# Kernel optimization log

Measured on AMD Instinct MI355X. Metric: run time of the kernel, lower is better.

Reference implementation:

```python
import jax, jax.numpy as jnp
import numpy as np

APPERTURE = 256
Q_SCALE = 0.06


def setup_inputs() -> dict:
    key = jax.random.key(0)
    ks = jax.random.split(key, 5)
    B, N, D_IN, D_OUT = 4, 4096, 1024, 1024
    std = 1.0 / np.sqrt(D_IN)
    x = jax.random.normal(ks[0], (B, N, D_IN), dtype=jnp.float32)
    Wk = jax.random.normal(ks[1], (D_OUT, D_IN), dtype=jnp.float32) * std
    Wq = jax.random.normal(ks[2], (D_OUT, D_IN), dtype=jnp.float32) * std
    Wv = jax.random.normal(ks[3], (D_OUT, D_IN), dtype=jnp.float32) * std
    Wo = jax.random.normal(ks[4], (D_IN, D_OUT), dtype=jnp.float32) * std
    return {"x": x, "Wk": Wk, "Wq": Wq, "Wv": Wv, "Wo": Wo}


def reference(x, Wk, Wq, Wv, Wo):
    # x: [B, N, D_in]; torch Linear(W) computes x @ W.T
    K = jnp.einsum('bnd,od->bno', x, Wk)          # [B, N, D_out]
    Q = jnp.einsum('bnd,od->bno', x, Wq) * Q_SCALE
    V = jnp.einsum('bnd,od->bno', x, Wv)
    logits = jnp.einsum('bno,bmo->bnm', Q, K)      # [B, N, N]
    N = x.shape[1]
    idx = jnp.arange(N)
    # tril(-a) + triu(a) masks |i-j| >= apperture (keep strict band)
    band_mask = jnp.abs(idx[:, None] - idx[None, :]) >= APPERTURE  # [N, N]
    logits = jnp.where(band_mask[None, :, :], -jnp.inf, logits)
    att_weights = jax.nn.softmax(logits, axis=-1)  # [B, N, N]
    # dropout is identity in eval mode
    # y = (V^T @ weights)^T  ->  y[b,n,:] = sum_m att[b,m,n] * V[b,m,:]
    y = jnp.einsum('bmn,bmo->bno', att_weights, V)
    y = jnp.einsum('bno,io->bni', y, Wo)           # [B, N, D_in]
    return (y, att_weights)
```

## Files before the change

kernel.cpp:

```cpp
#include <hip/hip_runtime.h>
#include <stdint.h>

#define SEQ 4096
#define DM  1024
#define NB  4
#define QSCALE 0.06f

typedef __attribute__((ext_vector_type(8))) short short8;
typedef __attribute__((ext_vector_type(4))) float floatx4;

__device__ __forceinline__ unsigned short f2bf(float f) {
  union { float f; unsigned int u; } v; v.f = f;
  unsigned int u = v.u;
  u += 0x7FFFu + ((u >> 16) & 1u);
  return (unsigned short)(u >> 16);
}

__device__ __forceinline__ void async16(const void* g, void* l) {
  __builtin_amdgcn_global_load_lds(
      (const __attribute__((address_space(1))) void*)g,
      (__attribute__((address_space(3))) void*)l, 16, 0, 0);
}

__global__ void cvt_bf16(const float* __restrict__ in,
                         unsigned short* __restrict__ out, int n) {
  int i = (blockIdx.x * 256 + threadIdx.x) * 8;
  if (i >= n) return;
  const float4* p = (const float4*)(in + i);
  float4 a = p[0], b = p[1];
  short8 o;
  o[0] = (short)f2bf(a.x); o[1] = (short)f2bf(a.y);
  o[2] = (short)f2bf(a.z); o[3] = (short)f2bf(a.w);
  o[4] = (short)f2bf(b.x); o[5] = (short)f2bf(b.y);
  o[6] = (short)f2bf(b.z); o[7] = (short)f2bf(b.w);
  *(short8*)(out + i) = o;
}

template <bool OUT_BF16, int MT>
__global__ __launch_bounds__(512, 2) void gemm256(
    const unsigned short* __restrict__ A, const unsigned short* __restrict__ W,
    void* __restrict__ Cout, float alpha, long ldc) {
  __shared__ __align__(16) unsigned short lds[4 * 16384];
  const int K = 1024;
  const int NKT = 32;
  int tid = threadIdx.x;
  int lane = tid & 63;
  int wid = tid >> 6;
  int wr = wid >> 2, wc = wid & 3;

  int bid = blockIdx.x;
  int raw = ((bid & 7) << 5) | (bid >> 3);
  int bx = raw % MT;
  int by = raw / MT;
  long brow = (long)bx * 256;
  long bcol = (long)by * 256;

  floatx4 acc[8][4];
#pragma unroll
  for (int i = 0; i < 8; i++)
#pragma unroll
    for (int j = 0; j < 4; j++) acc[i][j] = (floatx4){0.f, 0.f, 0.f, 0.f};

  const unsigned short* Ag = A + (brow + (tid >> 2)) * K + (tid & 3) * 8;
  const unsigned short* Wg = W + (bcol + (tid >> 2)) * K + (tid & 3) * 8;
  unsigned short* ldsW = lds + wid * 512;

  int aRd = (wr * 128 + (lane & 15)) * 32 + (lane >> 4) * 8;
  int bRd = (wc * 64 + (lane & 15)) * 32 + (lane >> 4) * 8;

#pragma unroll
  for (int tt = 0; tt < 3; tt++) {
    unsigned short* d = ldsW + tt * 16384;
    const unsigned short* a = Ag + tt * 32;
    const unsigned short* w = Wg + tt * 32;
    async16(a, d);
    async16(a + 128 * K, d + 4096);
    async16(w, d + 8192);
    async16(w + 128 * K, d + 12288);
  }
  asm volatile("s_waitcnt vmcnt(8)" ::: "memory");
  __builtin_amdgcn_s_barrier();

  for (int t = 0; t < NKT; ++t) {
    const unsigned short* bufA = lds + (t & 3) * 16384;
    const unsigned short* bufB = bufA + 8192;
    short8 a0[4], b0[4], a1[4];
#pragma unroll
    for (int mt = 0; mt < 4; mt++)
      a0[mt] = *(const short8*)(bufA + aRd + mt * 512);
#pragma unroll
    for (int nt = 0; nt < 4; nt++)
      b0[nt] = *(const short8*)(bufB + bRd + nt * 512);
    if (t + 3 < NKT) {
      unsigned short* d = ldsW + ((t + 3) & 3) * 16384;
      const unsigned short* a = Ag + (t + 3) * 32;
      async16(a, d);
      async16(a + 128 * K, d + 4096);
    }
    __builtin_amdgcn_s_barrier();
    __builtin_amdgcn_s_setprio(1);
#pragma unroll
    for (int mt = 0; mt < 4; mt++)
#pragma unroll
      for (int nt = 0; nt < 4; nt++)
        acc[mt][nt] = __builtin_amdgcn_mfma_f32_16x16x32_bf16(
            a0[mt], b0[nt], acc[mt][nt], 0, 0, 0);
    __builtin_amdgcn_s_setprio(0);
    __builtin_amdgcn_s_barrier();
#pragma unroll
    for (int mt = 0; mt < 4; mt++)
      a1[mt] = *(const short8*)(bufA + aRd + 2048 + mt * 512);
    if (t + 3 < NKT) {
      unsigned short* d = ldsW + ((t + 3) & 3) * 16384;
      const unsigned short* w = Wg + (t + 3) * 32;
      async16(w, d + 8192);
      async16(w + 128 * K, d + 12288);
    }
    __builtin_amdgcn_s_barrier();
    __builtin_amdgcn_s_setprio(1);
#pragma unroll
    for (int mt = 0; mt < 4; mt++)
#pragma unroll
      for (int nt = 0; nt < 4; nt++)
        acc[4 + mt][nt] = __builtin_amdgcn_mfma_f32_16x16x32_bf16(
            a1[mt], b0[nt], acc[4 + mt][nt], 0, 0, 0);
    __builtin_amdgcn_s_setprio(0);
    if (t < NKT - 3)
      asm volatile("s_waitcnt vmcnt(8)" ::: "memory");
    else if (t == NKT - 3)
      asm volatile("s_waitcnt vmcnt(4)" ::: "memory");
    else
      asm volatile("s_waitcnt vmcnt(0)" ::: "memory");
    __builtin_amdgcn_s_barrier();
  }

  long crow = brow + wr * 128 + (lane >> 4) * 4;
  long ccol = bcol + wc * 64 + (lane & 15);
#pragma unroll
  for (int mt = 0; mt < 8; mt++)
#pragma unroll
    for (int nt = 0; nt < 4; nt++)
#pragma unroll
      for (int r = 0; r < 4; r++) {
        float v = acc[mt][nt][r] * alpha;
        long idx = (crow + mt * 16 + r) * ldc + ccol + nt * 16;
        if (OUT_BF16)
          ((unsigned short*)Cout)[idx] = f2bf(v);
        else
          ((float*)Cout)[idx] = v;
      }
}

__global__ __launch_bounds__(256) void attn_logits(
    const unsigned short* __restrict__ Qb, const unsigned short* __restrict__ Kb,
    float* __restrict__ att) {
  int b = blockIdx.z;
  int n0 = blockIdx.y * 128;
  int m0 = n0 - 256 + blockIdx.x * 128;
  if (m0 + 128 <= 0 || m0 >= SEQ) return;
  __shared__ unsigned short sA[128 * 32];
  __shared__ unsigned short sB[128 * 32];
  const int K = 1024;
  int tid = threadIdx.x;
  int wid = tid >> 6, lane = tid & 63;
  int wr = wid >> 1, wc = wid & 1;

  floatx4 acc[4][4];
#pragma unroll
  for (int i = 0; i < 4; i++)
#pragma unroll
    for (int j = 0; j < 4; j++) acc[i][j] = (floatx4){0.f, 0.f, 0.f, 0.f};

  int c0 = wid * 64 + lane;
  int c1 = c0 + 256;
  const unsigned short* Qbase = Qb + (long)b * SEQ * K;
  const unsigned short* Kbase = Kb + (long)b * SEQ * K;
  int br0 = m0 + (c0 >> 2); br0 = br0 < 0 ? 0 : (br0 > SEQ - 1 ? SEQ - 1 : br0);
  int br1 = m0 + (c1 >> 2); br1 = br1 < 0 ? 0 : (br1 > SEQ - 1 ? SEQ - 1 : br1);
  const unsigned short* Ag0 = Qbase + (long)(n0 + (c0 >> 2)) * K + (c0 & 3) * 8;
  const unsigned short* Ag1 = Qbase + (long)(n0 + (c1 >> 2)) * K + (c1 & 3) * 8;
  const unsigned short* Bg0 = Kbase + (long)br0 * K + (c0 & 3) * 8;
  const unsigned short* Bg1 = Kbase + (long)br1 * K + (c1 & 3) * 8;
  unsigned short* sA0 = sA + (wid * 64) * 8;
  unsigned short* sA1 = sA + (256 + wid * 64) * 8;
  unsigned short* sB0 = sB + (wid * 64) * 8;
  unsigned short* sB1 = sB + (256 + wid * 64) * 8;

  int aRd = (wr * 64 + (lane & 15)) * 32 + (lane >> 4) * 8;
  int bRd = (wc * 64 + (lane & 15)) * 32 + (lane >> 4) * 8;

  for (int ks = 0; ks < K; ks += 32) {
    async16(Ag0 + ks, sA0);
    async16(Ag1 + ks, sA1);
    async16(Bg0 + ks, sB0);
    async16(Bg1 + ks, sB1);
    __syncthreads();
    short8 af[4], bf[4];
#pragma unroll
    for (int mt = 0; mt < 4; mt++) af[mt] = *(const short8*)(sA + aRd + mt * 512);
#pragma unroll
    for (int nt = 0; nt < 4; nt++) bf[nt] = *(const short8*)(sB + bRd + nt * 512);
#pragma unroll
    for (int mt = 0; mt < 4; mt++)
#pragma unroll
      for (int nt = 0; nt < 4; nt++)
        acc[mt][nt] = __builtin_amdgcn_mfma_f32_16x16x32_bf16(
            af[mt], bf[nt], acc[mt][nt], 0, 0, 0);
    __syncthreads();
  }

  float* attB = att + (long)b * SEQ * SEQ;
  int crow = n0 + wr * 64 + (lane >> 4) * 4;
  int ccol = m0 + wc * 64 + (lane & 15);
#pragma unroll
  for (int mt = 0; mt < 4; mt++)
#pragma unroll
    for (int nt = 0; nt < 4; nt++)
#pragma unroll
      for (int r = 0; r < 4; r++) {
        int row = crow + mt * 16 + r;
        int col = ccol + nt * 16;
        int d = row - col;
        if (col >= 0 && col < SEQ && d < 256 && d > -256)
          attB[(long)row * SEQ + col] = acc[mt][nt][r];
      }
}

__global__ __launch_bounds__(256) void softmax_band(
    float* __restrict__ att, unsigned short* __restrict__ attT2) {
  __shared__ float e_lds[16 * 545];
  __shared__ float inv_s[16];
  int blk = blockIdx.x;
  int b = blk >> 8;
  int r0 = (blk & 255) * 16;
  int tid = threadIdx.x;
  int row = tid >> 4;
  int t16 = tid & 15;
  int i = r0 + row;
  int jbase = r0 - 272;
  float* arow = att + ((long)b * SEQ + i) * (long)SEQ;

  float raw[34];
  float m = -1e30f;
#pragma unroll
  for (int s = 0; s < 34; s++) {
    int jj = s * 16 + t16;
    int j = jbase + jj;
    bool ok = (j >= 0) && (j < SEQ) && (j >= i - 255) && (j <= i + 255);
    float v = ok ? arow[j] : -1e30f;
    raw[s] = v;
    m = fmaxf(m, v);
  }
#pragma unroll
  for (int off = 8; off; off >>= 1) m = fmaxf(m, __shfl_xor(m, off, 16));

  float sum = 0.f;
#pragma unroll
  for (int s = 0; s < 34; s++) {
    int jj = s * 16 + t16;
    float e = (raw[s] > -1e29f) ? __expf(raw[s] - m) : 0.f;
    e_lds[row * 545 + jj] = e;
    sum += e;
  }
#pragma unroll
  for (int off = 8; off; off >>= 1) sum += __shfl_xor(sum, off, 16);
  float invr = 1.0f / sum;
  if (t16 == 0) inv_s[row] = invr;
  __syncthreads();

  for (int s = 0; s < 64; s++) {
    int j0 = (s * 16 + t16) * 4;
    float4 w;
    float* wp = (float*)&w;
#pragma unroll
    for (int k = 0; k < 4; k++) {
      int j = j0 + k;
      bool ok = (j >= i - 255) && (j <= i + 255);
      int jj = j - jbase;
      jj = jj < 0 ? 0 : (jj > 543 ? 543 : jj);
      wp[k] = ok ? e_lds[row * 545 + jj] * invr : 0.f;
    }
    *(float4*)(arow + j0) = w;
  }

  int nn = tid >> 4;
  int mi16 = tid & 15;
  int i2 = r0 + mi16;
  float inv2 = inv_s[mi16];
  for (int s = 0; s <= 32; s++) {
    int n = r0 - 256 + s * 16 + nn;
    if (n < 0 || n >= SEQ) continue;
    int N0b = n & ~127;
    int mi = i2 - N0b + 256;
    if (mi < 0 || mi >= 640) continue;
    bool ok = (n >= i2 - 255) && (n <= i2 + 255);
    int jj = n - jbase;
    float val = ok ? e_lds[mi16 * 545 + jj] * inv2 : 0.f;
    attT2[(((long)b * 32 + (N0b >> 7)) * 128 + (n & 127)) * 640 + mi] = f2bf(val);
  }
}

__global__ __launch_bounds__(256) void attv_gemm(
    const unsigned short* __restrict__ attT2, const unsigned short* __restrict__ Vt,
    unsigned short* __restrict__ yb) {
  __shared__ unsigned short sA[128 * 32];
  __shared__ unsigned short sB[128 * 32];
  const int KA = 640;
  int b = blockIdx.z;
  int tid = threadIdx.x;
  int wid = tid >> 6, lane = tid & 63;
  int wr = wid >> 1, wc = wid & 1;
  int N0 = blockIdx.x * 128;
  int o0 = blockIdx.y * 128;

  floatx4 acc[4][4];
#pragma unroll
  for (int i = 0; i < 4; i++)
#pragma unroll
    for (int j = 0; j < 4; j++) acc[i][j] = (floatx4){0.f, 0.f, 0.f, 0.f};

  int c0 = wid * 64 + lane;
  int c1 = c0 + 256;
  const unsigned short* Abase =
      attT2 + (((long)b * 32 + blockIdx.x) * 128) * KA;
  const unsigned short* Ag0 = Abase + (long)(c0 >> 2) * KA + (c0 & 3) * 8;
  const unsigned short* Ag1 = Abase + (long)(c1 >> 2) * KA + (c1 & 3) * 8;
  const unsigned short* Bg0 = Vt + (long)(o0 + (c0 >> 2)) * (NB * SEQ) + (c0 & 3) * 8;
  const unsigned short* Bg1 = Vt + (long)(o0 + (c1 >> 2)) * (NB * SEQ) + (c1 & 3) * 8;
  unsigned short* sA0 = sA + (wid * 64) * 8;
  unsigned short* sA1 = sA + (256 + wid * 64) * 8;
  unsigned short* sB0 = sB + (wid * 64) * 8;
  unsigned short* sB1 = sB + (256 + wid * 64) * 8;

  int aRd = (wr * 64 + (lane & 15)) * 32 + (lane >> 4) * 8;
  int bRd = (wc * 64 + (lane & 15)) * 32 + (lane >> 4) * 8;

  for (int ks = 0; ks < KA; ks += 32) {
    int mg = N0 - 256 + ks;
    int mc = mg < 0 ? 0 : (mg > SEQ - 32 ? SEQ - 32 : mg);
    long boff = (long)b * SEQ + mc;
    async16(Ag0 + ks, sA0);
    async16(Ag1 + ks, sA1);
    async16(Bg0 + boff, sB0);
    async16(Bg1 + boff, sB1);
    __syncthreads();
    short8 af[4], bf[4];
#pragma unroll
    for (int mt = 0; mt < 4; mt++) af[mt] = *(const short8*)(sA + aRd + mt * 512);
#pragma unroll
    for (int nt = 0; nt < 4; nt++) bf[nt] = *(const short8*)(sB + bRd + nt * 512);
#pragma unroll
    for (int mt = 0; mt < 4; mt++)
#pragma unroll
      for (int nt = 0; nt < 4; nt++)
        acc[mt][nt] = __builtin_amdgcn_mfma_f32_16x16x32_bf16(
            af[mt], bf[nt], acc[mt][nt], 0, 0, 0);
    __syncthreads();
  }

  long crow = (long)b * SEQ + N0 + wr * 64 + (lane >> 4) * 4;
  int ccol = o0 + wc * 64 + (lane & 15);
#pragma unroll
  for (int mt = 0; mt < 4; mt++)
#pragma unroll
    for (int nt = 0; nt < 4; nt++)
#pragma unroll
      for (int r = 0; r < 4; r++)
        yb[(crow + mt * 16 + r) * DM + ccol + nt * 16] = f2bf(acc[mt][nt][r]);
}

extern "C" void kernel_launch(void* const* d_in, const int* in_sizes, int n_in,
                              void* d_out, int out_size, void* d_ws, size_t ws_size,
                              hipStream_t stream) {
  const float* x  = (const float*)d_in[0];
  const float* Wk = (const float*)d_in[1];
  const float* Wq = (const float*)d_in[2];
  const float* Wv = (const float*)d_in[3];
  const float* Wo = (const float*)d_in[4];
  float* outY = (float*)d_out;
  float* outAtt = outY + (long)NB * SEQ * DM;

  char* ws = (char*)d_ws;
  unsigned short* xb  = (unsigned short*)(ws + 0);
  unsigned short* Kb  = (unsigned short*)(ws + 33554432);
  unsigned short* Qb  = (unsigned short*)(ws + 67108864);
  unsigned short* Vt  = (unsigned short*)(ws + 100663296);
  unsigned short* Wkb = (unsigned short*)(ws + 134217728);
  unsigned short* Wqb = Wkb + 1048576;
  unsigned short* Wvb = Wqb + 1048576;
  unsigned short* Wob = Wvb + 1048576;
  unsigned short* attT2 = Kb;
  unsigned short* yb = xb;

  cvt_bf16<<<8192, 256, 0, stream>>>(x, xb, NB * SEQ * DM);
  cvt_bf16<<<512, 256, 0, stream>>>(Wk, Wkb, DM * DM);
  cvt_bf16<<<512, 256, 0, stream>>>(Wq, Wqb, DM * DM);
  cvt_bf16<<<512, 256, 0, stream>>>(Wv, Wvb, DM * DM);
  cvt_bf16<<<512, 256, 0, stream>>>(Wo, Wob, DM * DM);

  gemm256<true, 64><<<256, 512, 0, stream>>>(xb, Wkb, Kb, 1.0f, 1024);
  gemm256<true, 64><<<256, 512, 0, stream>>>(xb, Wqb, Qb, QSCALE, 1024);
  gemm256<true, 4><<<256, 512, 0, stream>>>(Wvb, xb, Vt, 1.0f, NB * SEQ);

  attn_logits<<<dim3(5, 32, NB), 256, 0, stream>>>(Qb, Kb, outAtt);
  hipMemsetAsync(attT2, 0, (size_t)NB * 32 * 128 * 640 * 2, stream);
  softmax_band<<<1024, 256, 0, stream>>>(outAtt, attT2);
  attv_gemm<<<dim3(32, 8, NB), 256, 0, stream>>>(attT2, Vt, yb);
  gemm256<false, 64><<<256, 512, 0, stream>>>(yb, Wob, outY, 1.0f, 1024);
}
```

Measured before the change: 688.7 us.

## Fuse weight conversions and K/Q GEMMs; retile att·V to pipelined 256 blocks

Merges the four weight bf16 conversions into one launch and computes K and Q in a single GEMM over concatenated Wk|Wq, routing output columns to the right buffer with its own scale. Replaces the 128x128 single-buffered att·V GEMM with a 256x256, 512-thread, 4-stage async-pipelined kernel. The transposed attention layout changes to 256-row blocks with a 768-wide band, which adds about 20% more padded K-work per block. The intent is to cut launch overhead and improve MFMA utilisation and data reuse.

```diff
diff --git a/kernel.cpp b/kernel.cpp
--- a/kernel.cpp
+++ b/kernel.cpp
@@ -36,10 +36,27 @@
   *(short8*)(out + i) = o;
 }
 
-template <bool OUT_BF16, int MT>
+__global__ void cvt_w4(const float* __restrict__ wk, const float* __restrict__ wq,
+                       const float* __restrict__ wv, const float* __restrict__ wo,
+                       unsigned short* __restrict__ out) {
+  int blk = blockIdx.x;
+  int sel = blk >> 9;
+  const float* src = sel == 0 ? wk : sel == 1 ? wq : sel == 2 ? wv : wo;
+  int i = ((blk & 511) * 256 + threadIdx.x) * 8;
+  const float4* p = (const float4*)(src + i);
+  float4 a = p[0], b = p[1];
+  short8 o;
+  o[0] = (short)f2bf(a.x); o[1] = (short)f2bf(a.y);
+  o[2] = (short)f2bf(a.z); o[3] = (short)f2bf(a.w);
+  o[4] = (short)f2bf(b.x); o[5] = (short)f2bf(b.y);
+  o[6] = (short)f2bf(b.z); o[7] = (short)f2bf(b.w);
+  *(short8*)(out + sel * 1048576 + i) = o;
+}
+
+template <bool OUT_BF16, int MT, int NT, bool DUAL>
 __global__ __launch_bounds__(512, 2) void gemm256(
     const unsigned short* __restrict__ A, const unsigned short* __restrict__ W,
-    void* __restrict__ Cout, float alpha, long ldc) {
+    void* __restrict__ C0, void* __restrict__ C1, float a0, float a1, long ldc) {
   __shared__ __align__(16) unsigned short lds[4 * 16384];
   const int K = 1024;
   const int NKT = 32;
@@ -48,8 +65,9 @@
   int wid = tid >> 6;
   int wr = wid >> 2, wc = wid & 3;
 
+  const int CPX = (MT * NT) >> 3;
   int bid = blockIdx.x;
-  int raw = ((bid & 7) << 5) | (bid >> 3);
+  int raw = (bid & 7) * CPX + (bid >> 3);
   int bx = raw % MT;
   int by = raw / MT;
   long brow = (long)bx * 256;
@@ -84,13 +102,13 @@
   for (int t = 0; t < NKT; ++t) {
     const unsigned short* bufA = lds + (t & 3) * 16384;
     const unsigned short* bufB = bufA + 8192;
-    short8 a0[4], b0[4], a1[4];
-#pragma unroll
-    for (int mt = 0; mt < 4; mt++)
-      a0[mt] = *(const short8*)(bufA + aRd + mt * 512);
+    short8 a0f[4], b0f[4], a1f[4];
+#pragma unroll
+    for (int mt = 0; mt < 4; mt++)
+      a0f[mt] = *(const short8*)(bufA + aRd + mt * 512);
 #pragma unroll
     for (int nt = 0; nt < 4; nt++)
-      b0[nt] = *(const short8*)(bufB + bRd + nt * 512);
+      b0f[nt] = *(const short8*)(bufB + bRd + nt * 512);
     if (t + 3 < NKT) {
       unsigned short* d = ldsW + ((t + 3) & 3) * 16384;
       const unsigned short* a = Ag + (t + 3) * 32;
@@ -104,12 +122,12 @@
 #pragma unroll
       for (int nt = 0; nt < 4; nt++)
         acc[mt][nt] = __builtin_amdgcn_mfma_f32_16x16x32_bf16(
-            a0[mt], b0[nt], acc[mt][nt], 0, 0, 0);
+            a0f[mt], b0f[nt], acc[mt][nt], 0, 0, 0);
     __builtin_amdgcn_s_setprio(0);
     __builtin_amdgcn_s_barrier();
 #pragma unroll
     for (int mt = 0; mt < 4; mt++)
-      a1[mt] = *(const short8*)(bufA + aRd + 2048 + mt * 512);
+      a1f[mt] = *(const short8*)(bufA + aRd + 2048 + mt * 512);
     if (t + 3 < NKT) {
       unsigned short* d = ldsW + ((t + 3) & 3) * 16384;
       const unsigned short* w = Wg + (t + 3) * 32;
@@ -123,7 +141,7 @@
 #pragma unroll
       for (int nt = 0; nt < 4; nt++)
         acc[4 + mt][nt] = __builtin_amdgcn_mfma_f32_16x16x32_bf16(
-            a1[mt], b0[nt], acc[4 + mt][nt], 0, 0, 0);
+            a1f[mt], b0f[nt], acc[4 + mt][nt], 0, 0, 0);
     __builtin_amdgcn_s_setprio(0);
     if (t < NKT - 3)
       asm volatile("s_waitcnt vmcnt(8)" ::: "memory");
@@ -134,8 +152,16 @@
     __builtin_amdgcn_s_barrier();
   }
 
+  void* Cp;
+  float alpha;
+  long cc;
+  if (DUAL && by >= NT / 2) {
+    Cp = C1; alpha = a1; cc = bcol - (long)(NT / 2) * 256;
+  } else {
+    Cp = C0; alpha = a0; cc = bcol;
+  }
   long crow = brow + wr * 128 + (lane >> 4) * 4;
-  long ccol = bcol + wc * 64 + (lane & 15);
+  long ccol = cc + wc * 64 + (lane & 15);
 #pragma unroll
   for (int mt = 0; mt < 8; mt++)
 #pragma unroll
@@ -145,9 +171,9 @@
         float v = acc[mt][nt][r] * alpha;
         long idx = (crow + mt * 16 + r) * ldc + ccol + nt * 16;
         if (OUT_BF16)
-          ((unsigned short*)Cout)[idx] = f2bf(v);
+          ((unsigned short*)Cp)[idx] = f2bf(v);
         else
-          ((float*)Cout)[idx] = v;
+          ((float*)Cp)[idx] = v;
       }
 }
 
@@ -287,81 +313,123 @@
   int mi16 = tid & 15;
   int i2 = r0 + mi16;
   float inv2 = inv_s[mi16];
-  for (int s = 0; s <= 32; s++) {
-    int n = r0 - 256 + s * 16 + nn;
+  int Bc = r0 & ~255;
+  for (int s = 0; s < 48; s++) {
+    int n = Bc - 256 + s * 16 + nn;
     if (n < 0 || n >= SEQ) continue;
-    int N0b = n & ~127;
-    int mi = i2 - N0b + 256;
-    if (mi < 0 || mi >= 640) continue;
+    int mi = i2 - (n & ~255) + 256;
     bool ok = (n >= i2 - 255) && (n <= i2 + 255);
     int jj = n - jbase;
+    jj = jj < 0 ? 0 : (jj > 544 ? 544 : jj);
     float val = ok ? e_lds[mi16 * 545 + jj] * inv2 : 0.f;
-    attT2[(((long)b * 32 + (N0b >> 7)) * 128 + (n & 127)) * 640 + mi] = f2bf(val);
-  }
-}
-
-__global__ __launch_bounds__(256) void attv_gemm(
+    attT2[(((long)b * 16 + (n >> 8)) * 256 + (n & 255)) * 768 + mi] = f2bf(val);
+  }
+}
+
+__global__ __launch_bounds__(512, 2) void attv256(
     const unsigned short* __restrict__ attT2, const unsigned short* __restrict__ Vt,
     unsigned short* __restrict__ yb) {
-  __shared__ unsigned short sA[128 * 32];
-  __shared__ unsigned short sB[128 * 32];
-  const int KA = 640;
+  __shared__ __align__(16) unsigned short lds[4 * 16384];
+  const int KA = 768;
+  const int NKT = 24;
   int b = blockIdx.z;
+  int nb2 = blockIdx.x;
+  int o0 = blockIdx.y * 256;
+  int N0 = nb2 * 256;
   int tid = threadIdx.x;
-  int wid = tid >> 6, lane = tid & 63;
-  int wr = wid >> 1, wc = wid & 1;
-  int N0 = blockIdx.x * 128;
-  int o0 = blockIdx.y * 128;
-
-  floatx4 acc[4][4];
-#pragma unroll
-  for (int i = 0; i < 4; i++)
+  int lane = tid & 63;
+  int wid = tid >> 6;
+  int wr = wid >> 2, wc = wid & 3;
+
+  floatx4 acc[8][4];
+#pragma unroll
+  for (int i = 0; i < 8; i++)
 #pragma unroll
     for (int j = 0; j < 4; j++) acc[i][j] = (floatx4){0.f, 0.f, 0.f, 0.f};
 
-  int c0 = wid * 64 + lane;
-  int c1 = c0 + 256;
-  const unsigned short* Abase =
-      attT2 + (((long)b * 32 + blockIdx.x) * 128) * KA;
-  const unsigned short* Ag0 = Abase + (long)(c0 >> 2) * KA + (c0 & 3) * 8;
-  const unsigned short* Ag1 = Abase + (long)(c1 >> 2) * KA + (c1 & 3) * 8;
-  const unsigned short* Bg0 = Vt + (long)(o0 + (c0 >> 2)) * (NB * SEQ) + (c0 & 3) * 8;
-  const unsigned short* Bg1 = Vt + (long)(o0 + (c1 >> 2)) * (NB * SEQ) + (c1 & 3) * 8;
-  unsigned short* sA0 = sA + (wid * 64) * 8;
-  unsigned short* sA1 = sA + (256 + wid * 64) * 8;
-  unsigned short* sB0 = sB + (wid * 64) * 8;
-  unsigned short* sB1 = sB + (256 + wid * 64) * 8;
-
-  int aRd = (wr * 64 + (lane & 15)) * 32 + (lane >> 4) * 8;
+  const unsigned short* Abase = attT2 + ((long)(b * 16 + nb2) * 256) * KA;
+  const unsigned short* Ag = Abase + (long)(tid >> 2) * KA + (tid & 3) * 8;
+  const unsigned short* Vg =
+      Vt + (long)(o0 + (tid >> 2)) * (NB * SEQ) + (tid & 3) * 8;
+  unsigned short* ldsW = lds + wid * 512;
+
+  int aRd = (wr * 128 + (lane & 15)) * 32 + (lane >> 4) * 8;
   int bRd = (wc * 64 + (lane & 15)) * 32 + (lane >> 4) * 8;
 
-  for (int ks = 0; ks < KA; ks += 32) {
-    int mg = N0 - 256 + ks;
+  auto boff = [&](int t) {
+    int mg = N0 - 256 + t * 32;
     int mc = mg < 0 ? 0 : (mg > SEQ - 32 ? SEQ - 32 : mg);
-    long boff = (long)b * SEQ + mc;
-    async16(Ag0 + ks, sA0);
-    async16(Ag1 + ks, sA1);
-    async16(Bg0 + boff, sB0);
-    async16(Bg1 + boff, sB1);
-    __syncthreads();
-    short8 af[4], bf[4];
-#pragma unroll
-    for (int mt = 0; mt < 4; mt++) af[mt] = *(const short8*)(sA + aRd + mt * 512);
-#pragma unroll
-    for (int nt = 0; nt < 4; nt++) bf[nt] = *(const short8*)(sB + bRd + nt * 512);
+    return (long)b * SEQ + mc;
+  };
+
+#pragma unroll
+  for (int tt = 0; tt < 3; tt++) {
+    unsigned short* d = ldsW + tt * 16384;
+    async16(Ag + tt * 32, d);
+    async16(Ag + 128 * KA + tt * 32, d + 4096);
+    long bo = boff(tt);
+    async16(Vg + bo, d + 8192);
+    async16(Vg + 128L * (NB * SEQ) + bo, d + 12288);
+  }
+  asm volatile("s_waitcnt vmcnt(8)" ::: "memory");
+  __builtin_amdgcn_s_barrier();
+
+  for (int t = 0; t < NKT; ++t) {
+    const unsigned short* bufA = lds + (t & 3) * 16384;
+    const unsigned short* bufB = bufA + 8192;
+    short8 a0f[4], b0f[4], a1f[4];
+#pragma unroll
+    for (int mt = 0; mt < 4; mt++)
+      a0f[mt] = *(const short8*)(bufA + aRd + mt * 512);
+#pragma unroll
+    for (int nt = 0; nt < 4; nt++)
+      b0f[nt] = *(const short8*)(bufB + bRd + nt * 512);
+    if (t + 3 < NKT) {
+      unsigned short* d = ldsW + ((t + 3) & 3) * 16384;
+      async16(Ag + (t + 3) * 32, d);
+      async16(Ag + 128 * KA + (t + 3) * 32, d + 4096);
+    }
+    __builtin_amdgcn_s_barrier();
+    __builtin_amdgcn_s_setprio(1);
 #pragma unroll
     for (int mt = 0; mt < 4; mt++)
 #pragma unroll
       for (int nt = 0; nt < 4; nt++)
         acc[mt][nt] = __builtin_amdgcn_mfma_f32_16x16x32_bf16(
-            af[mt], bf[nt], acc[mt][nt], 0, 0, 0);
-    __syncthreads();
-  }
-
-  long crow = (long)b * SEQ + N0 + wr * 64 + (lane >> 4) * 4;
+            a0f[mt], b0f[nt], acc[mt][nt], 0, 0, 0);
+    __builtin_amdgcn_s_setprio(0);
+    __builtin_amdgcn_s_barrier();
+#pragma unroll
+    for (int mt = 0; mt < 4; mt++)
+      a1f[mt] = *(const short8*)(bufA + aRd + 2048 + mt * 512);
+    if (t + 3 < NKT) {
+      unsigned short* d = ldsW + ((t + 3) & 3) * 16384;
+      long bo = boff(t + 3);
+      async16(Vg + bo, d + 8192);
+      async16(Vg + 128L * (NB * SEQ) + bo, d + 12288);
+    }
+    __builtin_amdgcn_s_barrier();
+    __builtin_amdgcn_s_setprio(1);
+#pragma unroll
+    for (int mt = 0; mt < 4; mt++)
+#pragma unroll
+      for (int nt = 0; nt < 4; nt++)
+        acc[4 + mt][nt] = __builtin_amdgcn_mfma_f32_16x16x32_bf16(
+            a1f[mt], b0f[nt], acc[4 + mt][nt], 0, 0, 0);
+    __builtin_amdgcn_s_setprio(0);
+    if (t < NKT - 3)
+      asm volatile("s_waitcnt vmcnt(8)" ::: "memory");
+    else if (t == NKT - 3)
+      asm volatile("s_waitcnt vmcnt(4)" ::: "memory");
+    else
+      asm volatile("s_waitcnt vmcnt(0)" ::: "memory");
+    __builtin_amdgcn_s_barrier();
+  }
+
+  long crow = (long)b * SEQ + N0 + wr * 128 + (lane >> 4) * 4;
   int ccol = o0 + wc * 64 + (lane & 15);
 #pragma unroll
-  for (int mt = 0; mt < 4; mt++)
+  for (int mt = 0; mt < 8; mt++)
 #pragma unroll
     for (int nt = 0; nt < 4; nt++)
 #pragma unroll
@@ -386,25 +454,23 @@
   unsigned short* Qb  = (unsigned short*)(ws + 67108864);
   unsigned short* Vt  = (unsigned short*)(ws + 100663296);
   unsigned short* Wkb = (unsigned short*)(ws + 134217728);
-  unsigned short* Wqb = Wkb + 1048576;
-  unsigned short* Wvb = Wqb + 1048576;
+  unsigned short* Wvb = Wkb + 2097152;
   unsigned short* Wob = Wvb + 1048576;
   unsigned short* attT2 = Kb;
   unsigned short* yb = xb;
 
   cvt_bf16<<<8192, 256, 0, stream>>>(x, xb, NB * SEQ * DM);
-  cvt_bf16<<<512, 256, 0, stream>>>(Wk, Wkb, DM * DM);
-  cvt_bf16<<<512, 256, 0, stream>>>(Wq, Wqb, DM * DM);
-  cvt_bf16<<<512, 256, 0, stream>>>(Wv, Wvb, DM * DM);
-  cvt_bf16<<<512, 256, 0, stream>>>(Wo, Wob, DM * DM);
-
-  gemm256<true, 64><<<256, 512, 0, stream>>>(xb, Wkb, Kb, 1.0f, 1024);
-  gemm256<true, 64><<<256, 512, 0, stream>>>(xb, Wqb, Qb, QSCALE, 1024);
-  gemm256<true, 4><<<256, 512, 0, stream>>>(Wvb, xb, Vt, 1.0f, NB * SEQ);
+  cvt_w4<<<2048, 256, 0, stream>>>(Wk, Wq, Wv, Wo, Wkb);
+
+  gemm256<true, 64, 8, true><<<512, 512, 0, stream>>>(
+      xb, Wkb, Kb, Qb, 1.0f, QSCALE, 1024);
+  gemm256<true, 4, 64, false><<<256, 512, 0, stream>>>(
+      Wvb, xb, Vt, nullptr, 1.0f, 1.0f, NB * SEQ);
 
   attn_logits<<<dim3(5, 32, NB), 256, 0, stream>>>(Qb, Kb, outAtt);
-  hipMemsetAsync(attT2, 0, (size_t)NB * 32 * 128 * 640 * 2, stream);
+  hipMemsetAsync(attT2, 0, (size_t)NB * 16 * 256 * 768 * 2, stream);
   softmax_band<<<1024, 256, 0, stream>>>(outAtt, attT2);
-  attv_gemm<<<dim3(32, 8, NB), 256, 0, stream>>>(attT2, Vt, yb);
-  gemm256<false, 64><<<256, 512, 0, stream>>>(yb, Wob, outY, 1.0f, 1024);
-}
+  attv256<<<dim3(16, 4, NB), 512, 0, stream>>>(attT2, Vt, yb);
+  gemm256<false, 64, 4, false><<<256, 512, 0, stream>>>(
+      yb, Wob, outY, nullptr, 1.0f, 1.0f, 1024);
+}
```

Result: faster. 666.4 us (-3.2%).
